# Optimization experiments

Measured on AMD Instinct MI355X. Metric: run time of the kernel, lower is better.

## Reference

```python
import jax, jax.numpy as jnp
import numpy as np

B, T, C, H, M, O = 64, 2048, 256, 512, 512, 256
EPS = 1e-12


def retract(x):
    # Unit-sphere retraction: project onto the sphere (stand-in for the abstract Manifold).
    return x * jax.lax.rsqrt(jnp.sum(x * x, axis=-1, keepdims=True) + EPS)


def setup_inputs() -> dict:
    key = jax.random.key(0)
    ks = jax.random.split(key, 12)
    s = lambda k, shape, fan: jax.random.normal(k, shape, jnp.float32) / np.sqrt(fan).astype(np.float32)
    return {
        "control_values": jax.random.normal(ks[0], (B, T, C), jnp.float32),
        # initial-condition MLP (depth=2: in->M->M->H, softplus between hidden layers)
        "mlp_w0": s(ks[1], (M, C), C), "mlp_b0": jnp.zeros((M,), jnp.float32),
        "mlp_w1": s(ks[2], (M, M), M), "mlp_b1": jnp.zeros((M,), jnp.float32),
        "mlp_w2": s(ks[3], (H, M), M), "mlp_b2": jnp.zeros((H,), jnp.float32),
        # eqx.nn.GRUCell params
        "w_ih": s(ks[4], (3 * H, C), C), "w_hh": s(ks[5], (3 * H, H), H),
        "b": s(ks[6], (3 * H,), H), "b_n": s(ks[7], (H,), H),
        # readout Linear
        "w_out": s(ks[8], (O, H), H), "b_out": jnp.zeros((O,), jnp.float32),
    }


def reference(control_values, mlp_w0, mlp_b0, mlp_w1, mlp_b1, mlp_w2, mlp_b2,
              w_ih, w_hh, b, b_n, w_out, b_out):
    # Initial hidden state from MLP on x[0], then hidden-manifold retract.
    x0 = control_values[:, 0]                                  # (B, C)
    h = jax.nn.softplus(x0 @ mlp_w0.T + mlp_b0)                # (B, M)
    h = jax.nn.softplus(h @ mlp_w1.T + mlp_b1)                 # (B, M)
    h0 = retract(h @ mlp_w2.T + mlp_b2)                        # (B, H)

    xs = jnp.transpose(control_values[:, 1:], (1, 0, 2))       # (T-1, B, C)

    def step(hprev, xt):
        ig = xt @ w_ih.T + b                                   # (B, 3H)
        hg = hprev @ w_hh.T                                    # (B, 3H)
        ir, iz, inn = jnp.split(ig, 3, axis=-1)
        hr, hz, hn = jnp.split(hg, 3, axis=-1)
        r = jax.nn.sigmoid(ir + hr)
        z = jax.nn.sigmoid(iz + hz)
        n = jnp.tanh(inn + r * (hn + b_n))
        hnew = retract(n + z * (hprev - n))                    # GRU update + manifold retract
        return hnew, hnew

    _, hs_rest = jax.lax.scan(step, h0, xs)                    # (T-1, B, H)
    hs = jnp.concatenate([h0[None], hs_rest], axis=0)          # (T, B, H)

    # evolving_out=True: readout (identity activation) + manifold retract per step.
    y = retract(hs @ w_out.T + b_out)                          # (T, B, O)
    return jnp.transpose(y, (1, 0, 2))                         # (B, T, O)
```

## Files before the change

### kernel.cpp

```cpp
#include <hip/hip_runtime.h>
#include <math.h>

#define B_  64
#define T_  2048
#define C_  256
#define H_  512
#define O_  256
#define NSTEP 2047

typedef __attribute__((ext_vector_type(8))) short short8x;
typedef __attribute__((ext_vector_type(4))) float f32x4;

__device__ __forceinline__ unsigned short f2bf_bits(float x){
  unsigned int u = __builtin_bit_cast(unsigned int, x);
  u = u + 0x7FFFu + ((u >> 16) & 1u);
  return (unsigned short)(u >> 16);
}
__device__ __forceinline__ float bf2f(unsigned short h){
  unsigned int u = ((unsigned int)h) << 16;
  return __builtin_bit_cast(float, u);
}
__device__ __forceinline__ short8x pack8(float4 a, float4 b){
  short8x w;
  w[0]=(short)f2bf_bits(a.x); w[1]=(short)f2bf_bits(a.y);
  w[2]=(short)f2bf_bits(a.z); w[3]=(short)f2bf_bits(a.w);
  w[4]=(short)f2bf_bits(b.x); w[5]=(short)f2bf_bits(b.y);
  w[6]=(short)f2bf_bits(b.z); w[7]=(short)f2bf_bits(b.w);
  return w;
}
__device__ __forceinline__ f32x4 MFMA(short8x a, short8x b, f32x4 c){
  return __builtin_amdgcn_mfma_f32_16x16x32_bf16(a, b, c, 0, 0, 0);
}
__device__ __forceinline__ float softplus_f(float x){
  return (x > 20.f) ? x : log1pf(expf(x));
}
__device__ __forceinline__ float fast_exp2(float x){ return __builtin_amdgcn_exp2f(x); }
__device__ __forceinline__ float fast_rcp(float x){ return __builtin_amdgcn_rcpf(x); }
__device__ __forceinline__ float sigmoid_f(float x){
  return fast_rcp(1.f + fast_exp2(-1.44269504f * x));
}
__device__ __forceinline__ float tanh_f(float x){
  return 1.f - 2.f * fast_rcp(1.f + fast_exp2(2.88539008f * x));
}

__device__ __forceinline__ void st_agent_u32(unsigned* p, unsigned v){
  __hip_atomic_store(p, v, __ATOMIC_RELAXED, __HIP_MEMORY_SCOPE_AGENT);
}
__device__ __forceinline__ void st_agent_u16(unsigned short* p, unsigned short v){
  __hip_atomic_store(p, v, __ATOMIC_RELAXED, __HIP_MEMORY_SCOPE_AGENT);
}
__device__ __forceinline__ void st_agent_f32(float* p, float v){
  __hip_atomic_store(p, v, __ATOMIC_RELAXED, __HIP_MEMORY_SCOPE_AGENT);
}
__device__ __forceinline__ unsigned ld_agent_u32(unsigned* p){
  return __hip_atomic_load(p, __ATOMIC_RELAXED, __HIP_MEMORY_SCOPE_AGENT);
}
__device__ __forceinline__ float ld_agent_f32(float* p){
  return __hip_atomic_load(p, __ATOMIC_RELAXED, __HIP_MEMORY_SCOPE_AGENT);
}


__global__ void k_mlp(const float* __restrict__ cv,
                      const float* __restrict__ w0, const float* __restrict__ bb0,
                      const float* __restrict__ w1, const float* __restrict__ bb1,
                      const float* __restrict__ w2, const float* __restrict__ bb2,
                      unsigned short* __restrict__ hs, float* __restrict__ partials)
{
  const int b = blockIdx.x, tid = threadIdx.x;
  const int wave = tid >> 6, lane = tid & 63;
  __shared__ float xr[256], a0[512], a1[512], a2[512];
  __shared__ float red[4];

  xr[tid] = cv[(size_t)b * T_ * C_ + tid];
  __syncthreads();

  for (int i = 0; i < 32; i++){
    float s[4];
    #pragma unroll
    for (int uu = 0; uu < 4; uu++){
      int j = wave*128 + i*4 + uu;
      const float4* wr = (const float4*)(w0 + (size_t)j * 256);
      float4 w = wr[lane];
      s[uu] = w.x*xr[lane*4+0] + w.y*xr[lane*4+1] + w.z*xr[lane*4+2] + w.w*xr[lane*4+3];
    }
    #pragma unroll
    for (int off = 32; off; off >>= 1){
      #pragma unroll
      for (int uu = 0; uu < 4; uu++) s[uu] += __shfl_xor(s[uu], off, 64);
    }
    if (lane < 4){ int j = wave*128 + i*4 + lane; a0[j] = softplus_f(s[lane] + bb0[j]); }
  }
  __syncthreads();

  for (int i = 0; i < 32; i++){
    float s[4];
    #pragma unroll
    for (int uu = 0; uu < 4; uu++){
      int j = wave*128 + i*4 + uu;
      const float4* wr = (const float4*)(w1 + (size_t)j * 512);
      float4 wA = wr[lane*2], wB = wr[lane*2+1];
      int k0 = lane*8;
      s[uu] = wA.x*a0[k0]   + wA.y*a0[k0+1] + wA.z*a0[k0+2] + wA.w*a0[k0+3]
            + wB.x*a0[k0+4] + wB.y*a0[k0+5] + wB.z*a0[k0+6] + wB.w*a0[k0+7];
    }
    #pragma unroll
    for (int off = 32; off; off >>= 1){
      #pragma unroll
      for (int uu = 0; uu < 4; uu++) s[uu] += __shfl_xor(s[uu], off, 64);
    }
    if (lane < 4){ int j = wave*128 + i*4 + lane; a1[j] = softplus_f(s[lane] + bb1[j]); }
  }
  __syncthreads();

  for (int i = 0; i < 32; i++){
    float s[4];
    #pragma unroll
    for (int uu = 0; uu < 4; uu++){
      int j = wave*128 + i*4 + uu;
      const float4* wr = (const float4*)(w2 + (size_t)j * 512);
      float4 wA = wr[lane*2], wB = wr[lane*2+1];
      int k0 = lane*8;
      s[uu] = wA.x*a1[k0]   + wA.y*a1[k0+1] + wA.z*a1[k0+2] + wA.w*a1[k0+3]
            + wB.x*a1[k0+4] + wB.y*a1[k0+5] + wB.z*a1[k0+6] + wB.w*a1[k0+7];
    }
    #pragma unroll
    for (int off = 32; off; off >>= 1){
      #pragma unroll
      for (int uu = 0; uu < 4; uu++) s[uu] += __shfl_xor(s[uu], off, 64);
    }
    if (lane < 4){ int j = wave*128 + i*4 + lane; a2[j] = s[lane] + bb2[j]; }
  }
  __syncthreads();

  float sq = a2[tid]*a2[tid] + a2[tid+256]*a2[tid+256];
  #pragma unroll
  for (int off = 32; off; off >>= 1) sq += __shfl_xor(sq, off, 64);
  if (lane == 0) red[wave] = sq;
  __syncthreads();

  const int g = b >> 4, bb = b & 15;
  if (tid == 0)               partials[(size_t)g*512 + 0*32  + bb] = red[0]+red[1]+red[2]+red[3];
  if (tid >= 1 && tid < 16)   partials[(size_t)g*512 + tid*32 + bb] = 0.f;

  {
    int u = tid;
    hs[(size_t)g*8192 + (u>>5)*512 + bb*32 + (u&31)] = f2bf_bits(a2[u]);
    u = tid + 256;
    hs[(size_t)g*8192 + (u>>5)*512 + bb*32 + (u&31)] = f2bf_bits(a2[u]);
  }
}

__global__ void k_wcvt(const float* __restrict__ w, unsigned short* __restrict__ o)
{
  int idx = blockIdx.x * 256 + threadIdx.x;
  if (idx < O_ * H_) o[idx] = f2bf_bits(w[idx]);
}

__global__ __launch_bounds__(256, 1)
void k_scan(const float* __restrict__ cv, const float* __restrict__ w_ih,
            const float* __restrict__ w_hh, const float* __restrict__ bias,
            const float* __restrict__ b_n,
            unsigned short* __restrict__ hs, float* __restrict__ sumsq,
            unsigned* __restrict__ flags, float* __restrict__ partials)
{
  const int wg   = blockIdx.x;
  const int g    = wg >> 4;
  const int sidx = wg & 15;
  const int b0   = g * 16;
  const int u0   = sidx * 32;
  const int tid  = threadIdx.x;
  const int wave = tid >> 6, lane = tid & 63;
  const int lm   = lane & 15, quad = lane >> 4;
  const int gb   = tid >> 5;
  const int uu   = tid & 31;

  __shared__ float accLds[12][16][16];
  __shared__ float s_lds[16];
  __shared__ float bias_lds[3][32];
  __shared__ float bn_lds[32];

  if (tid < 32){
    bias_lds[0][tid] = bias[u0 + tid];
    bias_lds[1][tid] = bias[512 + u0 + tid];
    bias_lds[2][tid] = bias[1024 + u0 + tid];
    bn_lds[tid]      = b_n[u0 + tid];
  }
  float hp0 = bf2f(hs[(size_t)g*8192 + sidx*512 + gb*32 + uu]);
  float hp1 = bf2f(hs[(size_t)g*8192 + sidx*512 + (gb+8)*32 + uu]);

  short8x wreg[48];
  if (wave < 3){
    const int gate = wave;
    #pragma unroll
    for (int nt = 0; nt < 2; nt++){
      #pragma unroll
      for (int k = 0; k < 16; k++){
        const float* p = w_hh + ((size_t)(gate*512 + u0 + nt*16 + lm)) * 512 + k*32 + quad*8;
        wreg[nt*16 + k] = pack8(*(const float4*)p, *(const float4*)(p + 4));
      }
    }
  } else {
    #pragma unroll
    for (int g2 = 0; g2 < 3; g2++){
      #pragma unroll
      for (int nt = 0; nt < 2; nt++){
        #pragma unroll
        for (int kk = 0; kk < 8; kk++){
          const float* p = w_ih + ((size_t)(g2*512 + u0 + nt*16 + lm)) * 256 + kk*32 + quad*8;
          wreg[(g2*2 + nt)*8 + kk] = pack8(*(const float4*)p, *(const float4*)(p + 4));
        }
      }
    }
  }
  __syncthreads();

  unsigned* gflags = flags + g*32;

  for (int t = 1; t <= NSTEP; t++){
    const unsigned tgt = (unsigned)(t - 1);
    if (tid == 0) st_agent_u32(&gflags[sidx], tgt);

    if (wave < 3){
      for (;;){
        unsigned f = (lane < 16) ? ld_agent_u32(&gflags[lane]) : tgt;
        if (__all((int)(f >= tgt))) break;
      }
      asm volatile("" ::: "memory");
      const unsigned short* base = hs + ((size_t)(t-1)*4 + g)*8192 + lm*32 + quad*8;
      short8x af[16];
      #pragma unroll
      for (int k = 0; k < 16; k++)
        af[k] = *(const short8x*)(base + (size_t)k*512);
      f32x4 acc0 = {0.f,0.f,0.f,0.f}, acc1 = {0.f,0.f,0.f,0.f};
      #pragma unroll
      for (int k = 0; k < 16; k++){
        acc0 = MFMA(af[k], wreg[k],      acc0);
        acc1 = MFMA(af[k], wreg[16 + k], acc1);
      }
      #pragma unroll
      for (int r = 0; r < 4; r++){
        accLds[wave*2 + 0][quad*4 + r][lm] = acc0[r];
        accLds[wave*2 + 1][quad*4 + r][lm] = acc1[r];
      }
    } else {
      short8x af[8];
      const size_t xbase = ((size_t)(b0 + lm) * T_ + t) * C_;
      #pragma unroll
      for (int kk = 0; kk < 8; kk++){
        const float* xp = cv + xbase + kk*32 + quad*8;
        af[kk] = pack8(*(const float4*)xp, *(const float4*)(xp + 4));
      }
      f32x4 acc[6];
      #pragma unroll
      for (int tt = 0; tt < 6; tt++) acc[tt] = (f32x4){0.f,0.f,0.f,0.f};
      #pragma unroll
      for (int kk = 0; kk < 8; kk++){
        #pragma unroll
        for (int tt = 0; tt < 6; tt++) acc[tt] = MFMA(af[kk], wreg[tt*8 + kk], acc[tt]);
      }
      #pragma unroll
      for (int tt = 0; tt < 6; tt++){
        #pragma unroll
        for (int r = 0; r < 4; r++) accLds[6 + tt][quad*4 + r][lm] = acc[tt][r];
      }
      for (;;){
        unsigned f = (lane < 16) ? ld_agent_u32(&gflags[lane]) : tgt;
        if (__all((int)(f >= tgt))) break;
      }
      asm volatile("" ::: "memory");
      if (lane < 16){
        float* pp = partials + (size_t)((t-1)&1)*2048 + g*512 + lane;
        float v = 0.f;
        #pragma unroll
        for (int s = 0; s < 16; s++) v += ld_agent_f32(pp + s*32);
        if (sidx == 0) sumsq[(size_t)(t-1)*64 + b0 + lane] = v;
        s_lds[lane] = rsqrtf(v + 1e-12f);
      }
    }
    __syncthreads();

    const int nt = uu >> 4, ul = uu & 15;
    float sq0, sq1;
    {
      const float sp = s_lds[gb];
      float rv = accLds[6 + 0 + nt][gb][ul] + bias_lds[0][uu] + sp*accLds[0 + nt][gb][ul];
      float zv = accLds[6 + 2 + nt][gb][ul] + bias_lds[1][uu] + sp*accLds[2 + nt][gb][ul];
      float nv = accLds[6 + 4 + nt][gb][ul] + bias_lds[2][uu];
      float hn = sp*accLds[4 + nt][gb][ul];
      float r  = sigmoid_f(rv);
      float z  = sigmoid_f(zv);
      float n  = tanh_f(nv + r*(hn + bn_lds[uu]));
      float hp = sp * hp0;
      float hnew = n + z*(hp - n);
      hp0 = hnew;
      st_agent_u16(hs + ((size_t)t*4 + g)*8192 + sidx*512 + gb*32 + uu, f2bf_bits(hnew));
      sq0 = hnew * hnew;
    }
    {
      const float sp = s_lds[gb + 8];
      float rv = accLds[6 + 0 + nt][gb+8][ul] + bias_lds[0][uu] + sp*accLds[0 + nt][gb+8][ul];
      float zv = accLds[6 + 2 + nt][gb+8][ul] + bias_lds[1][uu] + sp*accLds[2 + nt][gb+8][ul];
      float nv = accLds[6 + 4 + nt][gb+8][ul] + bias_lds[2][uu];
      float hn = sp*accLds[4 + nt][gb+8][ul];
      float r  = sigmoid_f(rv);
      float z  = sigmoid_f(zv);
      float n  = tanh_f(nv + r*(hn + bn_lds[uu]));
      float hp = sp * hp1;
      float hnew = n + z*(hp - n);
      hp1 = hnew;
      st_agent_u16(hs + ((size_t)t*4 + g)*8192 + sidx*512 + (gb+8)*32 + uu, f2bf_bits(hnew));
      sq1 = hnew * hnew;
    }
    #pragma unroll
    for (int off = 16; off; off >>= 1){
      sq0 += __shfl_down(sq0, off, 32);
      sq1 += __shfl_down(sq1, off, 32);
    }
    if ((lane & 31) == 0){
      float* pb = partials + (size_t)(t&1)*2048 + g*512 + sidx*32;
      st_agent_f32(pb + gb,     sq0);
      st_agent_f32(pb + gb + 8, sq1);
    }
    __syncthreads();
  }

  if (tid == 0) st_agent_u32(&gflags[sidx], (unsigned)NSTEP);
  if (wave == 3 && sidx == 0){
    const unsigned tgt = (unsigned)NSTEP;
    for (;;){
      unsigned f = (lane < 16) ? ld_agent_u32(&gflags[lane]) : tgt;
      if (__all((int)(f >= tgt))) break;
    }
    asm volatile("" ::: "memory");
    if (lane < 16){
      float* pp = partials + (size_t)(NSTEP&1)*2048 + g*512 + lane;
      float v = 0.f;
      #pragma unroll
      for (int s = 0; s < 16; s++) v += ld_agent_f32(pp + s*32);
      sumsq[(size_t)NSTEP*64 + b0 + lane] = v;
    }
  }
}

__global__ __launch_bounds__(256, 2)
void k_ygemm(const unsigned short* __restrict__ hs, const float* __restrict__ sumsq,
             const unsigned short* __restrict__ wob, const float* __restrict__ b_out,
             float* __restrict__ out)
{
  const int t = blockIdx.x;
  const int tid = threadIdx.x, wave = tid >> 6, lane = tid & 63;
  const int lm = lane & 15, quad = lane >> 4;
  __shared__ float srow[64];
  __shared__ float bo[256];
  __shared__ float part[4][64];
  __shared__ float ysc[64];

  if (tid < 64) srow[tid] = rsqrtf(sumsq[(size_t)t*64 + tid] + 1e-12f);
  bo[tid] = b_out[tid];
  __syncthreads();

  f32x4 acc[4][4];
  #pragma unroll
  for (int mt = 0; mt < 4; mt++)
    #pragma unroll
    for (int nt = 0; nt < 4; nt++) acc[mt][nt] = (f32x4){0.f,0.f,0.f,0.f};

  const unsigned short* arow[4];
  const unsigned short* brow[4];
  #pragma unroll
  for (int mt = 0; mt < 4; mt++)
    arow[mt] = hs + ((size_t)t*4 + mt)*8192 + lm*32 + quad*8;
  #pragma unroll
  for (int nt = 0; nt < 4; nt++)
    brow[nt] = wob + ((size_t)(wave*64 + nt*16 + lm))*512 + quad*8;

  #pragma unroll 2
  for (int k = 0; k < 16; k++){
    short8x a[4], b[4];
    #pragma unroll
    for (int mt = 0; mt < 4; mt++) a[mt] = *(const short8x*)(arow[mt] + (size_t)k*512);
    #pragma unroll
    for (int nt = 0; nt < 4; nt++) b[nt] = *(const short8x*)(brow[nt] + k*32);
    #pragma unroll
    for (int mt = 0; mt < 4; mt++)
      #pragma unroll
      for (int nt = 0; nt < 4; nt++) acc[mt][nt] = MFMA(a[mt], b[nt], acc[mt][nt]);
  }

  float loc[4][4];
  #pragma unroll
  for (int mt = 0; mt < 4; mt++)
    #pragma unroll
    for (int r = 0; r < 4; r++) loc[mt][r] = 0.f;
  #pragma unroll
  for (int mt = 0; mt < 4; mt++){
    #pragma unroll
    for (int nt = 0; nt < 4; nt++){
      f32x4 v = acc[mt][nt];
      #pragma unroll
      for (int r = 0; r < 4; r++){
        int row = mt*16 + quad*4 + r;
        float y = srow[row]*v[r] + bo[wave*64 + nt*16 + lm];
        v[r] = y;
        loc[mt][r] += y*y;
      }
      acc[mt][nt] = v;
    }
  }
  #pragma unroll
  for (int off = 8; off; off >>= 1){
    #pragma unroll
    for (int mt = 0; mt < 4; mt++)
      #pragma unroll
      for (int r = 0; r < 4; r++) loc[mt][r] += __shfl_xor(loc[mt][r], off, 16);
  }
  if (lm == 0){
    #pragma unroll
    for (int mt = 0; mt < 4; mt++)
      #pragma unroll
      for (int r = 0; r < 4; r++) part[wave][mt*16 + quad*4 + r] = loc[mt][r];
  }
  __syncthreads();
  if (tid < 64) ysc[tid] = rsqrtf(part[0][tid] + part[1][tid] + part[2][tid] + part[3][tid] + 1e-12f);
  __syncthreads();

  #pragma unroll
  for (int mt = 0; mt < 4; mt++){
    #pragma unroll
    for (int nt = 0; nt < 4; nt++){
      #pragma unroll
      for (int r = 0; r < 4; r++){
        int row = mt*16 + quad*4 + r;
        int o   = wave*64 + nt*16 + lm;
        out[((size_t)row * T_ + t) * O_ + o] = acc[mt][nt][r] * ysc[row];
      }
    }
  }
}

extern "C" void kernel_launch(void* const* d_in, const int* in_sizes, int n_in,
                              void* d_out, int out_size, void* d_ws, size_t ws_size,
                              hipStream_t stream)
{
  (void)in_sizes; (void)n_in; (void)out_size;
  const float* cv   = (const float*)d_in[0];
  const float* w0   = (const float*)d_in[1];
  const float* b0v  = (const float*)d_in[2];
  const float* w1   = (const float*)d_in[3];
  const float* b1v  = (const float*)d_in[4];
  const float* w2   = (const float*)d_in[5];
  const float* b2v  = (const float*)d_in[6];
  const float* wih  = (const float*)d_in[7];
  const float* whh  = (const float*)d_in[8];
  const float* bg   = (const float*)d_in[9];
  const float* bn   = (const float*)d_in[10];
  const float* wout = (const float*)d_in[11];
  const float* bout = (const float*)d_in[12];
  float* out = (float*)d_out;

  const size_t HS_BYTES  = (size_t)T_ * B_ * H_ * 2;
  const size_t SS_BYTES  = (size_t)T_ * B_ * 4;
  const size_t OFF_SS    = HS_BYTES;
  const size_t OFF_FLG   = OFF_SS + SS_BYTES;
  const size_t OFF_PART  = OFF_FLG + 512;
  const size_t OFF_WOB   = OFF_PART + 16384;
  const size_t NEED      = OFF_WOB + (size_t)O_ * H_ * 2;
  if (ws_size < NEED) return;

  unsigned short* hs    = (unsigned short*)d_ws;
  float*          sumsq = (float*)((char*)d_ws + OFF_SS);
  unsigned*       flg   = (unsigned*)((char*)d_ws + OFF_FLG);
  float*          par   = (float*)((char*)d_ws + OFF_PART);
  unsigned short* wob   = (unsigned short*)((char*)d_ws + OFF_WOB);

  hipMemsetAsync((char*)d_ws + OFF_FLG, 0, 512, stream);
  hipLaunchKernelGGL(k_mlp,   dim3(64),   dim3(256), 0, stream,
                     cv, w0, b0v, w1, b1v, w2, b2v, hs, par);
  hipLaunchKernelGGL(k_wcvt,  dim3(512),  dim3(256), 0, stream, wout, wob);
  hipLaunchKernelGGL(k_scan,  dim3(64),   dim3(256), 0, stream,
                     cv, wih, whh, bg, bn, hs, sumsq, flg, par);
  hipLaunchKernelGGL(k_ygemm, dim3(2048), dim3(256), 0, stream,
                     hs, sumsq, wob, bout, out);
}
```

Before: 7.958 ms.

## Replace flag-based cross-block sync with sentinel-filled hidden-state polling

Removes the per-step flag stores/polls and the partial sum-of-squares exchange between workgroups. The hidden-state buffer is pre-filled with 0xFFFF sentinels, and consumers poll the bf16 data directly until no sentinel lane remains. Each workgroup then recomputes the row norm locally from the loaded bf16 values instead of reading published partials. This shortens the per-step critical path by dropping one round trip. It adds a large memset of the whole hidden-state buffer and relies on a real value never encoding as 0xFFFF (a NaN pattern) and on 64-bit atomic loads seeing consistent halves, and the norm now comes from rounded bf16 values.

```diff
diff --git a/kernel.cpp b/kernel.cpp
--- a/kernel.cpp
+++ b/kernel.cpp
@@ -43,20 +43,40 @@
   return 1.f - 2.f * fast_rcp(1.f + fast_exp2(2.88539008f * x));
 }
 
-__device__ __forceinline__ void st_agent_u32(unsigned* p, unsigned v){
-  __hip_atomic_store(p, v, __ATOMIC_RELAXED, __HIP_MEMORY_SCOPE_AGENT);
-}
 __device__ __forceinline__ void st_agent_u16(unsigned short* p, unsigned short v){
   __hip_atomic_store(p, v, __ATOMIC_RELAXED, __HIP_MEMORY_SCOPE_AGENT);
 }
-__device__ __forceinline__ void st_agent_f32(float* p, float v){
-  __hip_atomic_store(p, v, __ATOMIC_RELAXED, __HIP_MEMORY_SCOPE_AGENT);
-}
-__device__ __forceinline__ unsigned ld_agent_u32(unsigned* p){
+__device__ __forceinline__ unsigned long long ld_agent_u64(unsigned long long* p){
   return __hip_atomic_load(p, __ATOMIC_RELAXED, __HIP_MEMORY_SCOPE_AGENT);
 }
-__device__ __forceinline__ float ld_agent_f32(float* p){
-  return __hip_atomic_load(p, __ATOMIC_RELAXED, __HIP_MEMORY_SCOPE_AGENT);
+
+__device__ __forceinline__ int has_ffff(unsigned long long w){
+  unsigned long long nv = ~w;
+  return ((nv - 0x0001000100010001ull) & ~nv & 0x8000800080008000ull) != 0ull;
+}
+__device__ __forceinline__ float sq4(unsigned long long w){
+  unsigned lo = (unsigned)w, hi = (unsigned)(w >> 32);
+  float f0 = __builtin_bit_cast(float, lo << 16);
+  float f1 = __builtin_bit_cast(float, lo & 0xFFFF0000u);
+  float f2 = __builtin_bit_cast(float, hi << 16);
+  float f3 = __builtin_bit_cast(float, hi & 0xFFFF0000u);
+  return f0*f0 + f1*f1 + f2*f2 + f3*f3;
+}
+__device__ __forceinline__ short8x to8(unsigned long long w0, unsigned long long w1){
+  union { unsigned long long q[2]; short8x s; } u;
+  u.q[0] = w0; u.q[1] = w1;
+  return u.s;
+}
+
+__device__ __forceinline__ void barrier_lds(){
+  asm volatile("s_waitcnt lgkmcnt(0)" ::: "memory");
+  __builtin_amdgcn_s_barrier();
+  asm volatile("" ::: "memory");
+}
+__device__ __forceinline__ void barrier_exec(){
+  asm volatile("" ::: "memory");
+  __builtin_amdgcn_s_barrier();
+  asm volatile("" ::: "memory");
 }
 
 
@@ -64,12 +84,11 @@
                       const float* __restrict__ w0, const float* __restrict__ bb0,
                       const float* __restrict__ w1, const float* __restrict__ bb1,
                       const float* __restrict__ w2, const float* __restrict__ bb2,
-                      unsigned short* __restrict__ hs, float* __restrict__ partials)
+                      unsigned short* __restrict__ hs)
 {
   const int b = blockIdx.x, tid = threadIdx.x;
   const int wave = tid >> 6, lane = tid & 63;
   __shared__ float xr[256], a0[512], a1[512], a2[512];
-  __shared__ float red[4];
 
   xr[tid] = cv[(size_t)b * T_ * C_ + tid];
   __syncthreads();
@@ -132,16 +151,7 @@
   }
   __syncthreads();
 
-  float sq = a2[tid]*a2[tid] + a2[tid+256]*a2[tid+256];
-  #pragma unroll
-  for (int off = 32; off; off >>= 1) sq += __shfl_xor(sq, off, 64);
-  if (lane == 0) red[wave] = sq;
-  __syncthreads();
-
   const int g = b >> 4, bb = b & 15;
-  if (tid == 0)               partials[(size_t)g*512 + 0*32  + bb] = red[0]+red[1]+red[2]+red[3];
-  if (tid >= 1 && tid < 16)   partials[(size_t)g*512 + tid*32 + bb] = 0.f;
-
   {
     int u = tid;
     hs[(size_t)g*8192 + (u>>5)*512 + bb*32 + (u&31)] = f2bf_bits(a2[u]);
@@ -160,8 +170,7 @@
 void k_scan(const float* __restrict__ cv, const float* __restrict__ w_ih,
             const float* __restrict__ w_hh, const float* __restrict__ bias,
             const float* __restrict__ b_n,
-            unsigned short* __restrict__ hs, float* __restrict__ sumsq,
-            unsigned* __restrict__ flags, float* __restrict__ partials)
+            unsigned short* __restrict__ hs, float* __restrict__ sumsq)
 {
   const int wg   = blockIdx.x;
   const int g    = wg >> 4;
@@ -175,7 +184,7 @@
   const int uu   = tid & 31;
 
   __shared__ float accLds[12][16][16];
-  __shared__ float s_lds[16];
+  __shared__ float ssq[3][16];
   __shared__ float bias_lds[3][32];
   __shared__ float bn_lds[32];
 
@@ -214,34 +223,51 @@
   }
   __syncthreads();
 
-  unsigned* gflags = flags + g*32;
-
   for (int t = 1; t <= NSTEP; t++){
-    const unsigned tgt = (unsigned)(t - 1);
-    if (tid == 0) st_agent_u32(&gflags[sidx], tgt);
-
     if (wave < 3){
-      for (;;){
-        unsigned f = (lane < 16) ? ld_agent_u32(&gflags[lane]) : tgt;
-        if (__all((int)(f >= tgt))) break;
-      }
-      asm volatile("" ::: "memory");
-      const unsigned short* base = hs + ((size_t)(t-1)*4 + g)*8192 + lm*32 + quad*8;
-      short8x af[16];
-      #pragma unroll
-      for (int k = 0; k < 16; k++)
-        af[k] = *(const short8x*)(base + (size_t)k*512);
+      unsigned long long* base =
+        (unsigned long long*)(hs + ((size_t)(t-1)*4 + g)*8192 + lm*32 + quad*8);
+      unsigned long long v0[16], v1[16];
+      unsigned pend = 0xFFFFu;
+      do {
+        #pragma unroll
+        for (int k = 0; k < 16; k++){
+          if (pend & (1u<<k)){
+            v0[k] = ld_agent_u64(base + (size_t)k*128);
+            v1[k] = ld_agent_u64(base + (size_t)k*128 + 1);
+          }
+        }
+        unsigned np = 0u;
+        #pragma unroll
+        for (int k = 0; k < 16; k++){
+          if ((pend & (1u<<k)) && (has_ffff(v0[k]) | has_ffff(v1[k]))) np |= (1u<<k);
+        }
+        pend = np;
+      } while (__any((int)pend));
+
       f32x4 acc0 = {0.f,0.f,0.f,0.f}, acc1 = {0.f,0.f,0.f,0.f};
       #pragma unroll
       for (int k = 0; k < 16; k++){
-        acc0 = MFMA(af[k], wreg[k],      acc0);
-        acc1 = MFMA(af[k], wreg[16 + k], acc1);
+        short8x a = to8(v0[k], v1[k]);
+        acc0 = MFMA(a, wreg[k],      acc0);
+        acc1 = MFMA(a, wreg[16 + k], acc1);
       }
       #pragma unroll
       for (int r = 0; r < 4; r++){
         accLds[wave*2 + 0][quad*4 + r][lm] = acc0[r];
         accLds[wave*2 + 1][quad*4 + r][lm] = acc1[r];
       }
+
+      const int klo = (wave == 0) ? 0 : (wave == 1 ? 6 : 11);
+      const int khi = (wave == 0) ? 6 : (wave == 1 ? 11 : 16);
+      float s = 0.f;
+      #pragma unroll
+      for (int k = 0; k < 16; k++){
+        if (k >= klo && k < khi) s += sq4(v0[k]) + sq4(v1[k]);
+      }
+      s += __shfl_xor(s, 16, 64);
+      s += __shfl_xor(s, 32, 64);
+      if (lane < 16) ssq[wave][lane] = s;
     } else {
       short8x af[8];
       const size_t xbase = ((size_t)(b0 + lm) * T_ + t) * C_;
@@ -263,26 +289,18 @@
         #pragma unroll
         for (int r = 0; r < 4; r++) accLds[6 + tt][quad*4 + r][lm] = acc[tt][r];
       }
-      for (;;){
-        unsigned f = (lane < 16) ? ld_agent_u32(&gflags[lane]) : tgt;
-        if (__all((int)(f >= tgt))) break;
-      }
-      asm volatile("" ::: "memory");
-      if (lane < 16){
-        float* pp = partials + (size_t)((t-1)&1)*2048 + g*512 + lane;
-        float v = 0.f;
-        #pragma unroll
-        for (int s = 0; s < 16; s++) v += ld_agent_f32(pp + s*32);
-        if (sidx == 0) sumsq[(size_t)(t-1)*64 + b0 + lane] = v;
-        s_lds[lane] = rsqrtf(v + 1e-12f);
-      }
-    }
-    __syncthreads();
+    }
+    barrier_lds();
 
     const int nt = uu >> 4, ul = uu & 15;
-    float sq0, sq1;
+    const float s0 = ssq[0][gb]   + ssq[1][gb]   + ssq[2][gb];
+    const float s1 = ssq[0][gb+8] + ssq[1][gb+8] + ssq[2][gb+8];
+    if (sidx == 0 && uu == 0){
+      sumsq[(size_t)(t-1)*64 + b0 + gb]     = s0;
+      sumsq[(size_t)(t-1)*64 + b0 + gb + 8] = s1;
+    }
     {
-      const float sp = s_lds[gb];
+      const float sp = rsqrtf(s0 + 1e-12f);
       float rv = accLds[6 + 0 + nt][gb][ul] + bias_lds[0][uu] + sp*accLds[0 + nt][gb][ul];
       float zv = accLds[6 + 2 + nt][gb][ul] + bias_lds[1][uu] + sp*accLds[2 + nt][gb][ul];
       float nv = accLds[6 + 4 + nt][gb][ul] + bias_lds[2][uu];
@@ -294,10 +312,9 @@
       float hnew = n + z*(hp - n);
       hp0 = hnew;
       st_agent_u16(hs + ((size_t)t*4 + g)*8192 + sidx*512 + gb*32 + uu, f2bf_bits(hnew));
-      sq0 = hnew * hnew;
     }
     {
-      const float sp = s_lds[gb + 8];
+      const float sp = rsqrtf(s1 + 1e-12f);
       float rv = accLds[6 + 0 + nt][gb+8][ul] + bias_lds[0][uu] + sp*accLds[0 + nt][gb+8][ul];
       float zv = accLds[6 + 2 + nt][gb+8][ul] + bias_lds[1][uu] + sp*accLds[2 + nt][gb+8][ul];
       float nv = accLds[6 + 4 + nt][gb+8][ul] + bias_lds[2][uu];
@@ -309,36 +326,36 @@
       float hnew = n + z*(hp - n);
       hp1 = hnew;
       st_agent_u16(hs + ((size_t)t*4 + g)*8192 + sidx*512 + (gb+8)*32 + uu, f2bf_bits(hnew));
-      sq1 = hnew * hnew;
-    }
-    #pragma unroll
-    for (int off = 16; off; off >>= 1){
-      sq0 += __shfl_down(sq0, off, 32);
-      sq1 += __shfl_down(sq1, off, 32);
-    }
-    if ((lane & 31) == 0){
-      float* pb = partials + (size_t)(t&1)*2048 + g*512 + sidx*32;
-      st_agent_f32(pb + gb,     sq0);
-      st_agent_f32(pb + gb + 8, sq1);
-    }
-    __syncthreads();
-  }
-
-  if (tid == 0) st_agent_u32(&gflags[sidx], (unsigned)NSTEP);
-  if (wave == 3 && sidx == 0){
-    const unsigned tgt = (unsigned)NSTEP;
-    for (;;){
-      unsigned f = (lane < 16) ? ld_agent_u32(&gflags[lane]) : tgt;
-      if (__all((int)(f >= tgt))) break;
-    }
-    asm volatile("" ::: "memory");
-    if (lane < 16){
-      float* pp = partials + (size_t)(NSTEP&1)*2048 + g*512 + lane;
-      float v = 0.f;
-      #pragma unroll
-      for (int s = 0; s < 16; s++) v += ld_agent_f32(pp + s*32);
-      sumsq[(size_t)NSTEP*64 + b0 + lane] = v;
-    }
+    }
+    barrier_exec();
+  }
+
+  if (sidx == 0 && wave == 0){
+    unsigned long long* base =
+      (unsigned long long*)(hs + ((size_t)NSTEP*4 + g)*8192 + lm*32 + quad*8);
+    unsigned long long v0[16], v1[16];
+    unsigned pend = 0xFFFFu;
+    do {
+      #pragma unroll
+      for (int k = 0; k < 16; k++){
+        if (pend & (1u<<k)){
+          v0[k] = ld_agent_u64(base + (size_t)k*128);
+          v1[k] = ld_agent_u64(base + (size_t)k*128 + 1);
+        }
+      }
+      unsigned np = 0u;
+      #pragma unroll
+      for (int k = 0; k < 16; k++){
+        if ((pend & (1u<<k)) && (has_ffff(v0[k]) | has_ffff(v1[k]))) np |= (1u<<k);
+      }
+      pend = np;
+    } while (__any((int)pend));
+    float s = 0.f;
+    #pragma unroll
+    for (int k = 0; k < 16; k++) s += sq4(v0[k]) + sq4(v1[k]);
+    s += __shfl_xor(s, 16, 64);
+    s += __shfl_xor(s, 32, 64);
+    if (lane < 16) sumsq[(size_t)NSTEP*64 + b0 + lane] = s;
   }
 }
 
@@ -461,24 +478,22 @@
   const size_t HS_BYTES  = (size_t)T_ * B_ * H_ * 2;
   const size_t SS_BYTES  = (size_t)T_ * B_ * 4;
   const size_t OFF_SS    = HS_BYTES;
-  const size_t OFF_FLG   = OFF_SS + SS_BYTES;
-  const size_t OFF_PART  = OFF_FLG + 512;
-  const size_t OFF_WOB   = OFF_PART + 16384;
+  const size_t OFF_WOB   = OFF_SS + SS_BYTES;
   const size_t NEED      = OFF_WOB + (size_t)O_ * H_ * 2;
   if (ws_size < NEED) return;
 
   unsigned short* hs    = (unsigned short*)d_ws;
   float*          sumsq = (float*)((char*)d_ws + OFF_SS);
-  unsigned*       flg   = (unsigned*)((char*)d_ws + OFF_FLG);
-  float*          par   = (float*)((char*)d_ws + OFF_PART);
   unsigned short* wob   = (unsigned short*)((char*)d_ws + OFF_WOB);
 
-  hipMemsetAsync((char*)d_ws + OFF_FLG, 0, 512, stream);
+  const size_t T0_BYTES = (size_t)4 * 8192 * 2;
+  hipMemsetAsync((char*)d_ws + T0_BYTES, 0xFF, HS_BYTES - T0_BYTES, stream);
+
   hipLaunchKernelGGL(k_mlp,   dim3(64),   dim3(256), 0, stream,
-                     cv, w0, b0v, w1, b1v, w2, b2v, hs, par);
+                     cv, w0, b0v, w1, b1v, w2, b2v, hs);
   hipLaunchKernelGGL(k_wcvt,  dim3(512),  dim3(256), 0, stream, wout, wob);
   hipLaunchKernelGGL(k_scan,  dim3(64),   dim3(256), 0, stream,
-                     cv, wih, whh, bg, bn, hs, sumsq, flg, par);
+                     cv, wih, whh, bg, bn, hs, sumsq);
   hipLaunchKernelGGL(k_ygemm, dim3(2048), dim3(256), 0, stream,
                      hs, sumsq, wob, bout, out);
 }
```

Result: slower. 9.036 ms (+13.6%).
